# Performance work log

Hardware: AMD Instinct MI355X
Metric: run time of the kernel (lower is better)

Reference implementation:

```python
import jax, jax.numpy as jnp
import numpy as np

N_SRC = 100000   # source nodes
N_DST = 100000   # destination nodes
D = 128          # hidden_size (inner-product decoder)
E = 200000       # positive edges
NEG = 1000000    # E * neg_sampling_ratio (5)


def setup_inputs() -> dict:
    key = jax.random.key(0)
    k1, k2, k3, k4 = jax.random.split(key, 4)
    z_src = jax.random.normal(k1, (N_SRC, D), dtype=jnp.float32)
    z_dst = jax.random.normal(k2, (N_DST, D), dtype=jnp.float32)
    pos_edge_index = jnp.stack([
        jax.random.randint(k3, (E,), 0, N_SRC),
        jax.random.randint(jax.random.fold_in(k3, 1), (E,), 0, N_DST),
    ]).astype(jnp.int64)
    neg_edge_index = jnp.stack([
        jax.random.randint(k4, (NEG,), 0, N_SRC),
        jax.random.randint(jax.random.fold_in(k4, 1), (NEG,), 0, N_DST),
    ]).astype(jnp.int64)
    return {
        "z_src": z_src,
        "z_dst": z_dst,
        "pos_edge_index": pos_edge_index,
        "neg_edge_index": neg_edge_index,
    }


def reference(z_src, z_dst, pos_edge_index, neg_edge_index):
    # Inner-product edge decoder: logit = <z_src[u], z_dst[v]>
    pos_logits = jnp.sum(z_src[pos_edge_index[0]] * z_dst[pos_edge_index[1]], axis=-1)  # [E]
    neg_logits = jnp.sum(z_src[neg_edge_index[0]] * z_dst[neg_edge_index[1]], axis=-1)  # [NEG]
    # BCE-with-logits: target=1 -> softplus(-x); target=0 -> softplus(x)
    pos_loss = jnp.mean(jax.nn.softplus(-pos_logits))
    neg_loss = jnp.mean(jax.nn.softplus(neg_logits))
    return (pos_loss + neg_loss) * 0.5
```

## Files before the change

### kernel.cpp

```cpp
#include <hip/hip_runtime.h>
#include <hip/hip_fp16.h>
#include <math.h>


#define DIM 128
#define LPE 16

typedef _Float16 hf2 __attribute__((ext_vector_type(2)));

__device__ __forceinline__ float softplus_fast(float x) {
    const float t = __expf(-fabsf(x));
    return fmaxf(x, 0.0f) + __logf(1.0f + t);
}

__device__ __forceinline__ float dot8h(uint4 a, uint4 b, float acc) {
#if __has_builtin(__builtin_amdgcn_fdot2)
    const hf2* pa = (const hf2*)&a;
    const hf2* pb = (const hf2*)&b;
    #pragma unroll
    for (int j = 0; j < 4; ++j)
        acc = __builtin_amdgcn_fdot2(pa[j], pb[j], acc, false);
#else
    const __half2* ha = (const __half2*)&a;
    const __half2* hb = (const __half2*)&b;
    #pragma unroll
    for (int j = 0; j < 4; ++j) {
        const float2 fa = __half22float2(ha[j]);
        const float2 fb = __half22float2(hb[j]);
        acc = fmaf(fa.x, fb.x, acc);
        acc = fmaf(fa.y, fb.y, acc);
    }
#endif
    return acc;
}

__device__ __forceinline__ bool probe_wide(const void* idx) {
    const unsigned* p = (const unsigned*)idx;
    unsigned ored = 0;
    #pragma unroll
    for (int i = 0; i < 8; ++i) ored |= p[2 * i + 1];
    return ored == 0;
}

__device__ __forceinline__ void load_uv(const void* idx, bool wide, int e, int stride,
                                        int& u, int& v) {
    if (wide) {
        const long long* p = (const long long*)idx;
        u = (int)p[e]; v = (int)p[stride + e];
    } else {
        const int* p = (const int*)idx;
        u = p[e]; v = p[stride + e];
    }
}

__global__ __launch_bounds__(256) void convert_kernel(
        const float* __restrict__ srcf, const float* __restrict__ dstf,
        __half* __restrict__ srch, __half* __restrict__ dsth,
        int nsrc, int ndst, double* __restrict__ accum) {
    if (blockIdx.x == 0 && threadIdx.x == 0) { accum[0] = 0.0; accum[1] = 0.0; }
    const int tid    = blockIdx.x * blockDim.x + threadIdx.x;
    const int stride = gridDim.x * blockDim.x;
    const int total8 = (nsrc + ndst) / 8;
    union H8 { uint4 u; __half h[8]; };
    for (int i = tid; i < total8; i += stride) {
        const bool is_src = (i < nsrc / 8);
        const int  j      = is_src ? i : i - nsrc / 8;
        const float4* p   = (const float4*)(is_src ? srcf : dstf) + 2 * (size_t)j;
        const float4 a = p[0], b = p[1];
        H8 o;
        o.h[0] = __float2half_rn(a.x); o.h[1] = __float2half_rn(a.y);
        o.h[2] = __float2half_rn(a.z); o.h[3] = __float2half_rn(a.w);
        o.h[4] = __float2half_rn(b.x); o.h[5] = __float2half_rn(b.y);
        o.h[6] = __float2half_rn(b.z); o.h[7] = __float2half_rn(b.w);
        ((uint4*)(is_src ? srch : dsth))[j] = o.u;
    }
}

__global__ __launch_bounds__(256) void edge_loss_h_kernel(
        const __half* __restrict__ zs, const __half* __restrict__ zd,
        const void* __restrict__ pos_idx, const void* __restrict__ neg_idx,
        int E, int NEG, double* __restrict__ accum) {
    const bool wide    = probe_wide(pos_idx);
    const int  sub     = threadIdx.x & (LPE - 1);
    const int  group   = (blockIdx.x * blockDim.x + threadIdx.x) >> 4;
    const int  ngroups = (gridDim.x * blockDim.x) >> 4;
    const int  total   = E + NEG;

    float pos_acc = 0.0f, neg_acc = 0.0f;

    for (int e0 = group; e0 < total; e0 += 4 * ngroups) {
        int u0 = 0, v0 = 0, u1 = 0, v1 = 0, u2 = 0, v2 = 0, u3 = 0, v3 = 0;
        const int e1 = e0 + ngroups, e2 = e0 + 2 * ngroups, e3 = e0 + 3 * ngroups;
        if (e0 < E) load_uv(pos_idx, wide, e0, E, u0, v0);
        else        load_uv(neg_idx, wide, e0 - E, NEG, u0, v0);
        if (e1 < total) {
            if (e1 < E) load_uv(pos_idx, wide, e1, E, u1, v1);
            else        load_uv(neg_idx, wide, e1 - E, NEG, u1, v1);
        }
        if (e2 < total) {
            if (e2 < E) load_uv(pos_idx, wide, e2, E, u2, v2);
            else        load_uv(neg_idx, wide, e2 - E, NEG, u2, v2);
        }
        if (e3 < total) {
            if (e3 < E) load_uv(pos_idx, wide, e3, E, u3, v3);
            else        load_uv(neg_idx, wide, e3 - E, NEG, u3, v3);
        }
        const uint4 a0 = ((const uint4*)(zs + (size_t)u0 * DIM))[sub];
        const uint4 b0 = ((const uint4*)(zd + (size_t)v0 * DIM))[sub];
        const uint4 a1 = ((const uint4*)(zs + (size_t)u1 * DIM))[sub];
        const uint4 b1 = ((const uint4*)(zd + (size_t)v1 * DIM))[sub];
        const uint4 a2 = ((const uint4*)(zs + (size_t)u2 * DIM))[sub];
        const uint4 b2 = ((const uint4*)(zd + (size_t)v2 * DIM))[sub];
        const uint4 a3 = ((const uint4*)(zs + (size_t)u3 * DIM))[sub];
        const uint4 b3 = ((const uint4*)(zd + (size_t)v3 * DIM))[sub];
        float p0 = dot8h(a0, b0, 0.0f);
        float p1 = dot8h(a1, b1, 0.0f);
        float p2 = dot8h(a2, b2, 0.0f);
        float p3 = dot8h(a3, b3, 0.0f);
        #pragma unroll
        for (int off = 8; off > 0; off >>= 1) {
            p0 += __shfl_xor(p0, off);
            p1 += __shfl_xor(p1, off);
            p2 += __shfl_xor(p2, off);
            p3 += __shfl_xor(p3, off);
        }
        {
            const bool ip = (e0 < E);
            const float s = softplus_fast(ip ? -p0 : p0);
            if (ip) pos_acc += s; else neg_acc += s;
        }
        if (e1 < total) {
            const bool ip = (e1 < E);
            const float s = softplus_fast(ip ? -p1 : p1);
            if (ip) pos_acc += s; else neg_acc += s;
        }
        if (e2 < total) {
            const bool ip = (e2 < E);
            const float s = softplus_fast(ip ? -p2 : p2);
            if (ip) pos_acc += s; else neg_acc += s;
        }
        if (e3 < total) {
            const bool ip = (e3 < E);
            const float s = softplus_fast(ip ? -p3 : p3);
            if (ip) pos_acc += s; else neg_acc += s;
        }
    }

    #pragma unroll
    for (int off = 32; off > 0; off >>= 1) {
        pos_acc += __shfl_down(pos_acc, off);
        neg_acc += __shfl_down(neg_acc, off);
    }
    __shared__ float sp[4], sn[4];
    const int wid = threadIdx.x >> 6, lane = threadIdx.x & 63;
    if (lane == 0) { sp[wid] = pos_acc; sn[wid] = neg_acc; }
    __syncthreads();
    if (threadIdx.x == 0) {
        float ps = 0.0f, ns = 0.0f;
        #pragma unroll
        for (int i = 0; i < 4; ++i) { ps += sp[i]; ns += sn[i]; }
        atomicAdd(&accum[0], (double)ps);
        atomicAdd(&accum[1], (double)ns);
    }
}

__global__ void zero_accum_kernel(double* accum) { accum[0] = 0.0; accum[1] = 0.0; }

__global__ __launch_bounds__(256) void edge_loss_f_kernel(
        const float* __restrict__ zs, const float* __restrict__ zd,
        const void* __restrict__ pos_idx, const void* __restrict__ neg_idx,
        int E, int NEG, double* __restrict__ accum) {
    const bool wide    = probe_wide(pos_idx);
    const int  sub     = threadIdx.x & (LPE - 1);
    const int  group   = (blockIdx.x * blockDim.x + threadIdx.x) >> 4;
    const int  ngroups = (gridDim.x * blockDim.x) >> 4;
    const int  total   = E + NEG;
    float pos_acc = 0.0f, neg_acc = 0.0f;
    for (int e = group; e < total; e += ngroups) {
        const bool is_pos = (e < E);
        int u, v;
        if (is_pos) load_uv(pos_idx, wide, e, E, u, v);
        else        load_uv(neg_idx, wide, e - E, NEG, u, v);
        const float4* srow = (const float4*)zs + (size_t)u * (DIM / 4);
        const float4* drow = (const float4*)zd + (size_t)v * (DIM / 4);
        const float4 a0 = srow[sub], a1 = srow[sub + LPE];
        const float4 b0 = drow[sub], b1 = drow[sub + LPE];
        float p = a0.x * b0.x + a0.y * b0.y + a0.z * b0.z + a0.w * b0.w
                + a1.x * b1.x + a1.y * b1.y + a1.z * b1.z + a1.w * b1.w;
        #pragma unroll
        for (int off = 8; off > 0; off >>= 1) p += __shfl_xor(p, off);
        const float s = softplus_fast(is_pos ? -p : p);
        if (is_pos) pos_acc += s; else neg_acc += s;
    }
    #pragma unroll
    for (int off = 32; off > 0; off >>= 1) {
        pos_acc += __shfl_down(pos_acc, off);
        neg_acc += __shfl_down(neg_acc, off);
    }
    __shared__ float sp[4], sn[4];
    const int wid = threadIdx.x >> 6, lane = threadIdx.x & 63;
    if (lane == 0) { sp[wid] = pos_acc; sn[wid] = neg_acc; }
    __syncthreads();
    if (threadIdx.x == 0) {
        float ps = 0.0f, ns = 0.0f;
        #pragma unroll
        for (int i = 0; i < 4; ++i) { ps += sp[i]; ns += sn[i]; }
        atomicAdd(&accum[0], (double)ps);
        atomicAdd(&accum[1], (double)ns);
    }
}

__global__ void edge_loss_finalize(const double* __restrict__ accum,
                                   float* __restrict__ out, int E, int NEG) {
    const double inv = 1.0 / (double)LPE;
    out[0] = (float)((accum[0] * inv / (double)E + accum[1] * inv / (double)NEG) * 0.5);
}

extern "C" void kernel_launch(void* const* d_in, const int* in_sizes, int n_in,
                              void* d_out, int out_size, void* d_ws, size_t ws_size,
                              hipStream_t stream) {
    const float* z_src   = (const float*)d_in[0];
    const float* z_dst   = (const float*)d_in[1];
    const void*  pos_idx = d_in[2];
    const void*  neg_idx = d_in[3];
    const int E   = in_sizes[2] / 2;
    const int NEG = in_sizes[3] / 2;
    float*  out   = (float*)d_out;
    double* accum = (double*)d_ws;

    const size_t nsrc = (size_t)in_sizes[0], ndst = (size_t)in_sizes[1];
    const size_t need = 256 + (nsrc + ndst) * sizeof(__half);

    if (ws_size >= need) {
        __half* zs_h = (__half*)((char*)d_ws + 256);
        __half* zd_h = zs_h + nsrc;
        convert_kernel<<<2048, 256, 0, stream>>>(z_src, z_dst, zs_h, zd_h,
                                                 (int)nsrc, (int)ndst, accum);
        edge_loss_h_kernel<<<2048, 256, 0, stream>>>(zs_h, zd_h, pos_idx, neg_idx,
                                                     E, NEG, accum);
    } else {
        zero_accum_kernel<<<1, 1, 0, stream>>>(accum);
        edge_loss_f_kernel<<<2048, 256, 0, stream>>>(z_src, z_dst, pos_idx, neg_idx,
                                                     E, NEG, accum);
    }
    edge_loss_finalize<<<1, 1, 0, stream>>>(accum, out, E, NEG);
}
```

Measured before the change: 235.9 us.

## Quantize embeddings to int8 with per-row scales and use sdot4 dot products

Replaces the fp16 staging of the embedding tables with per-row symmetric int8 quantization plus a float scale per row. The edge kernel then gathers 128-byte rows with 8 lanes per edge and computes dot products with packed int8 dot instructions, rescaling by the two row scales. This halves the gather traffic per edge compared with fp16, at the cost of two extra scale loads per edge and a loss of precision in the logits that may exceed the tolerance.

Result: faster. 216.1 us (-8.4%).

```diff
diff --git a/kernel.cpp b/kernel.cpp
--- a/kernel.cpp
+++ b/kernel.cpp
@@ -1,37 +1,37 @@
 #include <hip/hip_runtime.h>
-#include <hip/hip_fp16.h>
 #include <math.h>
 
 
 #define DIM 128
-#define LPE 16
-
-typedef _Float16 hf2 __attribute__((ext_vector_type(2)));
+#define QLPE 8
+#define CLPE 16
 
 __device__ __forceinline__ float softplus_fast(float x) {
     const float t = __expf(-fabsf(x));
     return fmaxf(x, 0.0f) + __logf(1.0f + t);
 }
 
-__device__ __forceinline__ float dot8h(uint4 a, uint4 b, float acc) {
-#if __has_builtin(__builtin_amdgcn_fdot2)
-    const hf2* pa = (const hf2*)&a;
-    const hf2* pb = (const hf2*)&b;
-    #pragma unroll
-    for (int j = 0; j < 4; ++j)
-        acc = __builtin_amdgcn_fdot2(pa[j], pb[j], acc, false);
+__device__ __forceinline__ int dot4i8(int a, int b, int c) {
+#if __has_builtin(__builtin_amdgcn_sdot4)
+    return __builtin_amdgcn_sdot4(a, b, c, false);
 #else
-    const __half2* ha = (const __half2*)&a;
-    const __half2* hb = (const __half2*)&b;
-    #pragma unroll
-    for (int j = 0; j < 4; ++j) {
-        const float2 fa = __half22float2(ha[j]);
-        const float2 fb = __half22float2(hb[j]);
-        acc = fmaf(fa.x, fb.x, acc);
-        acc = fmaf(fa.y, fb.y, acc);
-    }
+    #pragma unroll
+    for (int k = 0; k < 4; ++k) {
+        const int av = (int)(signed char)(a >> (8 * k));
+        const int bv = (int)(signed char)(b >> (8 * k));
+        c += av * bv;
+    }
+    return c;
 #endif
-    return acc;
+}
+
+__device__ __forceinline__ int dot16i8(uint4 a, uint4 b) {
+    int c = 0;
+    c = dot4i8((int)a.x, (int)b.x, c);
+    c = dot4i8((int)a.y, (int)b.y, c);
+    c = dot4i8((int)a.z, (int)b.z, c);
+    c = dot4i8((int)a.w, (int)b.w, c);
+    return c;
 }
 
 __device__ __forceinline__ bool probe_wide(const void* idx) {
@@ -53,37 +53,51 @@
     }
 }
 
-__global__ __launch_bounds__(256) void convert_kernel(
+__global__ __launch_bounds__(256) void convert_q_kernel(
         const float* __restrict__ srcf, const float* __restrict__ dstf,
-        __half* __restrict__ srch, __half* __restrict__ dsth,
-        int nsrc, int ndst, double* __restrict__ accum) {
+        signed char* __restrict__ qs, signed char* __restrict__ qd,
+        float* __restrict__ ss, float* __restrict__ sd,
+        int rs, int rd, double* __restrict__ accum) {
     if (blockIdx.x == 0 && threadIdx.x == 0) { accum[0] = 0.0; accum[1] = 0.0; }
-    const int tid    = blockIdx.x * blockDim.x + threadIdx.x;
-    const int stride = gridDim.x * blockDim.x;
-    const int total8 = (nsrc + ndst) / 8;
-    union H8 { uint4 u; __half h[8]; };
-    for (int i = tid; i < total8; i += stride) {
-        const bool is_src = (i < nsrc / 8);
-        const int  j      = is_src ? i : i - nsrc / 8;
-        const float4* p   = (const float4*)(is_src ? srcf : dstf) + 2 * (size_t)j;
-        const float4 a = p[0], b = p[1];
-        H8 o;
-        o.h[0] = __float2half_rn(a.x); o.h[1] = __float2half_rn(a.y);
-        o.h[2] = __float2half_rn(a.z); o.h[3] = __float2half_rn(a.w);
-        o.h[4] = __float2half_rn(b.x); o.h[5] = __float2half_rn(b.y);
-        o.h[6] = __float2half_rn(b.z); o.h[7] = __float2half_rn(b.w);
-        ((uint4*)(is_src ? srch : dsth))[j] = o.u;
-    }
-}
-
-__global__ __launch_bounds__(256) void edge_loss_h_kernel(
-        const __half* __restrict__ zs, const __half* __restrict__ zd,
+    const int sub     = threadIdx.x & (CLPE - 1);
+    const int group   = (blockIdx.x * blockDim.x + threadIdx.x) >> 4;
+    const int ngroups = (gridDim.x * blockDim.x) >> 4;
+    const int total   = rs + rd;
+    for (int r = group; r < total; r += ngroups) {
+        const bool is_src = (r < rs);
+        const int  j      = is_src ? r : r - rs;
+        const float4* row = (const float4*)(is_src ? srcf : dstf) + (size_t)j * (DIM / 4);
+        const float4 a = row[sub];
+        const float4 b = row[sub + CLPE];
+        float m = fmaxf(fmaxf(fmaxf(fabsf(a.x), fabsf(a.y)), fmaxf(fabsf(a.z), fabsf(a.w))),
+                        fmaxf(fmaxf(fabsf(b.x), fabsf(b.y)), fmaxf(fabsf(b.z), fabsf(b.w))));
+        #pragma unroll
+        for (int off = 8; off > 0; off >>= 1)
+            m = fmaxf(m, __shfl_xor(m, off));
+        const float inv = (m > 0.0f) ? (127.0f / m) : 0.0f;
+        int q[8];
+        q[0] = __float2int_rn(a.x * inv); q[1] = __float2int_rn(a.y * inv);
+        q[2] = __float2int_rn(a.z * inv); q[3] = __float2int_rn(a.w * inv);
+        q[4] = __float2int_rn(b.x * inv); q[5] = __float2int_rn(b.y * inv);
+        q[6] = __float2int_rn(b.z * inv); q[7] = __float2int_rn(b.w * inv);
+        uint2 packed;
+        packed.x = (q[0] & 255) | ((q[1] & 255) << 8) | ((q[2] & 255) << 16) | ((unsigned)(q[3] & 255) << 24);
+        packed.y = (q[4] & 255) | ((q[5] & 255) << 8) | ((q[6] & 255) << 16) | ((unsigned)(q[7] & 255) << 24);
+        signed char* qrow = (is_src ? qs : qd) + (size_t)j * DIM;
+        ((uint2*)qrow)[sub] = packed;
+        if (sub == 0) (is_src ? ss : sd)[j] = (m > 0.0f) ? (m / 127.0f) : 0.0f;
+    }
+}
+
+__global__ __launch_bounds__(256) void edge_loss_q_kernel(
+        const signed char* __restrict__ qs, const signed char* __restrict__ qd,
+        const float* __restrict__ ss, const float* __restrict__ sd,
         const void* __restrict__ pos_idx, const void* __restrict__ neg_idx,
         int E, int NEG, double* __restrict__ accum) {
     const bool wide    = probe_wide(pos_idx);
-    const int  sub     = threadIdx.x & (LPE - 1);
-    const int  group   = (blockIdx.x * blockDim.x + threadIdx.x) >> 4;
-    const int  ngroups = (gridDim.x * blockDim.x) >> 4;
+    const int  sub     = threadIdx.x & (QLPE - 1);
+    const int  group   = (blockIdx.x * blockDim.x + threadIdx.x) >> 3;
+    const int  ngroups = (gridDim.x * blockDim.x) >> 3;
     const int  total   = E + NEG;
 
     float pos_acc = 0.0f, neg_acc = 0.0f;
@@ -105,43 +119,47 @@
             if (e3 < E) load_uv(pos_idx, wide, e3, E, u3, v3);
             else        load_uv(neg_idx, wide, e3 - E, NEG, u3, v3);
         }
-        const uint4 a0 = ((const uint4*)(zs + (size_t)u0 * DIM))[sub];
-        const uint4 b0 = ((const uint4*)(zd + (size_t)v0 * DIM))[sub];
-        const uint4 a1 = ((const uint4*)(zs + (size_t)u1 * DIM))[sub];
-        const uint4 b1 = ((const uint4*)(zd + (size_t)v1 * DIM))[sub];
-        const uint4 a2 = ((const uint4*)(zs + (size_t)u2 * DIM))[sub];
-        const uint4 b2 = ((const uint4*)(zd + (size_t)v2 * DIM))[sub];
-        const uint4 a3 = ((const uint4*)(zs + (size_t)u3 * DIM))[sub];
-        const uint4 b3 = ((const uint4*)(zd + (size_t)v3 * DIM))[sub];
-        float p0 = dot8h(a0, b0, 0.0f);
-        float p1 = dot8h(a1, b1, 0.0f);
-        float p2 = dot8h(a2, b2, 0.0f);
-        float p3 = dot8h(a3, b3, 0.0f);
-        #pragma unroll
-        for (int off = 8; off > 0; off >>= 1) {
-            p0 += __shfl_xor(p0, off);
-            p1 += __shfl_xor(p1, off);
-            p2 += __shfl_xor(p2, off);
-            p3 += __shfl_xor(p3, off);
+        const uint4 a0 = ((const uint4*)(qs + (size_t)u0 * DIM))[sub];
+        const uint4 b0 = ((const uint4*)(qd + (size_t)v0 * DIM))[sub];
+        const uint4 a1 = ((const uint4*)(qs + (size_t)u1 * DIM))[sub];
+        const uint4 b1 = ((const uint4*)(qd + (size_t)v1 * DIM))[sub];
+        const uint4 a2 = ((const uint4*)(qs + (size_t)u2 * DIM))[sub];
+        const uint4 b2 = ((const uint4*)(qd + (size_t)v2 * DIM))[sub];
+        const uint4 a3 = ((const uint4*)(qs + (size_t)u3 * DIM))[sub];
+        const uint4 b3 = ((const uint4*)(qd + (size_t)v3 * DIM))[sub];
+        int i0 = dot16i8(a0, b0);
+        int i1 = dot16i8(a1, b1);
+        int i2 = dot16i8(a2, b2);
+        int i3 = dot16i8(a3, b3);
+        #pragma unroll
+        for (int off = 4; off > 0; off >>= 1) {
+            i0 += __shfl_xor(i0, off);
+            i1 += __shfl_xor(i1, off);
+            i2 += __shfl_xor(i2, off);
+            i3 += __shfl_xor(i3, off);
         }
         {
+            const float p = (float)i0 * (ss[u0] * sd[v0]);
             const bool ip = (e0 < E);
-            const float s = softplus_fast(ip ? -p0 : p0);
+            const float s = softplus_fast(ip ? -p : p);
             if (ip) pos_acc += s; else neg_acc += s;
         }
         if (e1 < total) {
+            const float p = (float)i1 * (ss[u1] * sd[v1]);
             const bool ip = (e1 < E);
-            const float s = softplus_fast(ip ? -p1 : p1);
+            const float s = softplus_fast(ip ? -p : p);
             if (ip) pos_acc += s; else neg_acc += s;
         }
         if (e2 < total) {
+            const float p = (float)i2 * (ss[u2] * sd[v2]);
             const bool ip = (e2 < E);
-            const float s = softplus_fast(ip ? -p2 : p2);
+            const float s = softplus_fast(ip ? -p : p);
             if (ip) pos_acc += s; else neg_acc += s;
         }
         if (e3 < total) {
+            const float p = (float)i3 * (ss[u3] * sd[v3]);
             const bool ip = (e3 < E);
-            const float s = softplus_fast(ip ? -p3 : p3);
+            const float s = softplus_fast(ip ? -p : p);
             if (ip) pos_acc += s; else neg_acc += s;
         }
     }
@@ -171,7 +189,7 @@
         const void* __restrict__ pos_idx, const void* __restrict__ neg_idx,
         int E, int NEG, double* __restrict__ accum) {
     const bool wide    = probe_wide(pos_idx);
-    const int  sub     = threadIdx.x & (LPE - 1);
+    const int  sub     = threadIdx.x & (CLPE - 1);
     const int  group   = (blockIdx.x * blockDim.x + threadIdx.x) >> 4;
     const int  ngroups = (gridDim.x * blockDim.x) >> 4;
     const int  total   = E + NEG;
@@ -183,8 +201,8 @@
         else        load_uv(neg_idx, wide, e - E, NEG, u, v);
         const float4* srow = (const float4*)zs + (size_t)u * (DIM / 4);
         const float4* drow = (const float4*)zd + (size_t)v * (DIM / 4);
-        const float4 a0 = srow[sub], a1 = srow[sub + LPE];
-        const float4 b0 = drow[sub], b1 = drow[sub + LPE];
+        const float4 a0 = srow[sub], a1 = srow[sub + CLPE];
+        const float4 b0 = drow[sub], b1 = drow[sub + CLPE];
         float p = a0.x * b0.x + a0.y * b0.y + a0.z * b0.z + a0.w * b0.w
                 + a1.x * b1.x + a1.y * b1.y + a1.z * b1.z + a1.w * b1.w;
         #pragma unroll
@@ -211,9 +229,10 @@
 }
 
 __global__ void edge_loss_finalize(const double* __restrict__ accum,
-                                   float* __restrict__ out, int E, int NEG) {
-    const double inv = 1.0 / (double)LPE;
-    out[0] = (float)((accum[0] * inv / (double)E + accum[1] * inv / (double)NEG) * 0.5);
+                                   float* __restrict__ out, int E, int NEG,
+                                   double inv_lanes) {
+    out[0] = (float)((accum[0] * inv_lanes / (double)E +
+                      accum[1] * inv_lanes / (double)NEG) * 0.5);
 }
 
 extern "C" void kernel_launch(void* const* d_in, const int* in_sizes, int n_in,
@@ -228,20 +247,24 @@
     float*  out   = (float*)d_out;
     double* accum = (double*)d_ws;
 
-    const size_t nsrc = (size_t)in_sizes[0], ndst = (size_t)in_sizes[1];
-    const size_t need = 256 + (nsrc + ndst) * sizeof(__half);
+    const int rs = in_sizes[0] / DIM;
+    const int rd = in_sizes[1] / DIM;
+    const size_t need = 256 + (size_t)(rs + rd) * DIM + (size_t)(rs + rd) * 4;
 
     if (ws_size >= need) {
-        __half* zs_h = (__half*)((char*)d_ws + 256);
-        __half* zd_h = zs_h + nsrc;
-        convert_kernel<<<2048, 256, 0, stream>>>(z_src, z_dst, zs_h, zd_h,
-                                                 (int)nsrc, (int)ndst, accum);
-        edge_loss_h_kernel<<<2048, 256, 0, stream>>>(zs_h, zd_h, pos_idx, neg_idx,
+        signed char* qs = (signed char*)d_ws + 256;
+        signed char* qd = qs + (size_t)rs * DIM;
+        float* ss = (float*)(qd + (size_t)rd * DIM);
+        float* sd = ss + rs;
+        convert_q_kernel<<<2048, 256, 0, stream>>>(z_src, z_dst, qs, qd, ss, sd,
+                                                   rs, rd, accum);
+        edge_loss_q_kernel<<<2048, 256, 0, stream>>>(qs, qd, ss, sd, pos_idx, neg_idx,
                                                      E, NEG, accum);
+        edge_loss_finalize<<<1, 1, 0, stream>>>(accum, out, E, NEG, 1.0 / QLPE);
     } else {
         zero_accum_kernel<<<1, 1, 0, stream>>>(accum);
         edge_loss_f_kernel<<<2048, 256, 0, stream>>>(z_src, z_dst, pos_idx, neg_idx,
                                                      E, NEG, accum);
-    }
-    edge_loss_finalize<<<1, 1, 0, stream>>>(accum, out, E, NEG);
-}
+        edge_loss_finalize<<<1, 1, 0, stream>>>(accum, out, E, NEG, 1.0 / CLPE);
+    }
+}
```
